# Optimization experiments

Hardware: AMD Instinct MI355X
Metric: run time of the kernel (lower is better)

Reference implementation:

```python
import jax, jax.numpy as jnp
import numpy as np

LAMBDA_GEO = 0.5


def setup_inputs() -> dict:
    key = jax.random.key(0)
    embeddings = jax.random.normal(key, (4, 2048, 512), dtype=jnp.float32)
    return {"embeddings": embeddings}


def _geometric_loss(embeddings):
    b, s, d = embeddings.shape
    x = embeddings.reshape(b * s, d)  # [N, d]
    sq_norm = jnp.sum(x * x, axis=-1)  # [N]
    sq = sq_norm[:, None] + sq_norm[None, :] - 2.0 * (x @ x.T)  # [N, N]
    sq = jnp.maximum(sq, 0.0)
    dist = jnp.sqrt(sq)  # torch.cdist(p=2)
    return jnp.mean(jnp.exp(-dist * 0.1)) * 0.1


def reference(embeddings):
    geometric_loss = _geometric_loss(embeddings)
    total_geometric = LAMBDA_GEO * geometric_loss
    return geometric_loss, total_geometric
```

## Files before the change

### kernel.cpp

```cpp
#include <hip/hip_runtime.h>

#define NROWS 8192
#define DIM   512
#define NT    64
#define NTRI  (NT * (NT + 1) / 2)
#define NACC  64

using f32x4 = __attribute__((ext_vector_type(4))) float;

__device__ __forceinline__ unsigned char f2e4m3(float x) {
    unsigned ux = __float_as_uint(x);
    unsigned s  = (ux >> 24) & 0x80u;
    float a = __uint_as_float(ux & 0x7FFFFFFFu);
    a = fminf(a, 448.0f);
    unsigned ua = __float_as_uint(a);
    int eb = (int)(ua >> 23);
    if (eb < 121) eb = 121;
    float step  = __uint_as_float((unsigned)(eb - 3) << 23);
    float istep = __uint_as_float((unsigned)(257 - eb) << 23);
    float q = rintf(a * istep) * step;
    q = fminf(q, 448.0f);
    if (q < 0.001953125f)
        return (unsigned char)s;
    unsigned uq = __float_as_uint(q);
    int eq = (int)(uq >> 23) - 127;
    unsigned byte;
    if (eq < -6) byte = (unsigned)(q * 512.0f);
    else         byte = (unsigned)((eq + 7) << 3) | ((uq >> 20) & 7u);
    return (unsigned char)(s | byte);
}

__global__ __launch_bounds__(256) void norm_convert_kernel(
    const float* __restrict__ X, unsigned char* __restrict__ Xq,
    float* __restrict__ norms, float* __restrict__ acc)
{
    const int tid  = threadIdx.x;
    const int lane = tid & 63;
    const int w    = tid >> 6;
    const int row  = blockIdx.x * 4 + w;

    if (blockIdx.x == 0 && tid < NACC) acc[tid] = 0.0f;

    const float* xr = X + (size_t)row * DIM + lane * 8;
    float4 v0 = *(const float4*)xr;
    float4 v1 = *(const float4*)(xr + 4);

    float s = 0.0f;
    s = fmaf(v0.x, v0.x, s); s = fmaf(v0.y, v0.y, s);
    s = fmaf(v0.z, v0.z, s); s = fmaf(v0.w, v0.w, s);
    s = fmaf(v1.x, v1.x, s); s = fmaf(v1.y, v1.y, s);
    s = fmaf(v1.z, v1.z, s); s = fmaf(v1.w, v1.w, s);

    union { unsigned char b[8]; uint2 v; } pk;
    pk.b[0] = f2e4m3(v0.x); pk.b[1] = f2e4m3(v0.y);
    pk.b[2] = f2e4m3(v0.z); pk.b[3] = f2e4m3(v0.w);
    pk.b[4] = f2e4m3(v1.x); pk.b[5] = f2e4m3(v1.y);
    pk.b[6] = f2e4m3(v1.z); pk.b[7] = f2e4m3(v1.w);

    const int slab = lane >> 2;
    const int cpos = (lane & 3) ^ ((row >> 2) & 3);
    *(uint2*)(Xq + (size_t)row * DIM + slab * 32 + cpos * 8) = pk.v;

    #pragma unroll
    for (int off = 32; off > 0; off >>= 1) s += __shfl_down(s, off, 64);
    if (lane == 0) norms[row] = s;
}

__global__ __launch_bounds__(256, 4) void pair_loss_gemm_kernel(
    const unsigned char* __restrict__ Xq, const float* __restrict__ norms,
    float* __restrict__ acc)
{
    __shared__ __align__(16) char As0[4096];
    __shared__ __align__(16) char As1[4096];
    __shared__ __align__(16) char Bs0[4096];
    __shared__ __align__(16) char Bs1[4096];
    __shared__ float wsum[4];

    int t = blockIdx.x, bi = 0;
    while (t >= (NT - bi)) { t -= (NT - bi); bi++; }
    const int bj = bi + t;

    const int tid  = threadIdx.x;
    const int lane = tid & 63;
    const int w    = tid >> 6;

    const int rowA = bi * 128;
    const int rowB = bj * 128;

    f32x4 accv[4][4];
    const f32x4 zero = {0.0f, 0.0f, 0.0f, 0.0f};
    #pragma unroll
    for (int a = 0; a < 4; a++)
        #pragma unroll
        for (int b = 0; b < 4; b++) accv[a][b] = zero;

    const int r0 = tid >> 1;
    const int h0 = tid & 1;
    const int wb = r0 * 32 + h0 * 16;
    const unsigned char* gA = Xq + (size_t)(rowA + r0) * DIM + h0 * 16;
    const unsigned char* gB = Xq + (size_t)(rowB + r0) * DIM + h0 * 16;

    const int fr = lane & 15;
    const int q  = lane >> 4;
    const int fo = fr * 32 + (q ^ ((fr >> 2) & 3)) * 8;
    const int wr = (w & 1) * 64;
    const int wc = (w >> 1) * 64;

    {
        uint4 pa = *(const uint4*)gA;
        uint4 pb = *(const uint4*)gB;
        *(uint4*)(As0 + wb) = pa;
        *(uint4*)(Bs0 + wb) = pb;
    }
    __syncthreads();

    char* curA = As0; char* nxtA = As1;
    char* curB = Bs0; char* nxtB = Bs1;

    #pragma unroll 1
    for (int k = 0; k < 16; k++) {
        uint4 pa, pb;
        const bool more = (k < 15);
        if (more) {
            const int k0 = (k + 1) * 32;
            pa = *(const uint4*)(gA + k0);
            pb = *(const uint4*)(gB + k0);
        }

        long af[4], bf[4];
        #pragma unroll
        for (int a = 0; a < 4; a++)
            af[a] = *(const long*)(curA + (wr + a * 16) * 32 + fo);
        #pragma unroll
        for (int b = 0; b < 4; b++)
            bf[b] = *(const long*)(curB + (wc + b * 16) * 32 + fo);

        #pragma unroll
        for (int a = 0; a < 4; a++)
            #pragma unroll
            for (int b = 0; b < 4; b++)
                accv[a][b] = __builtin_amdgcn_mfma_f32_16x16x32_fp8_fp8(
                    af[a], bf[b], accv[a][b], 0, 0, 0);

        if (more) {
            *(uint4*)(nxtA + wb) = pa;
            *(uint4*)(nxtB + wb) = pb;
            __syncthreads();
            char* tA = curA; curA = nxtA; nxtA = tA;
            char* tB = curB; curB = nxtB; nxtB = tB;
        }
    }

    const float wgt = (bi == bj) ? 1.0f : 2.0f;
    float lsum = 0.0f;
    #pragma unroll
    for (int a = 0; a < 4; a++) {
        const int gi0 = rowA + wr + a * 16 + (lane >> 4) * 4;
        #pragma unroll
        for (int b = 0; b < 4; b++) {
            const int gj = rowB + wc + b * 16 + (lane & 15);
            const float nj = norms[gj];
            #pragma unroll
            for (int r = 0; r < 4; r++) {
                const int gi = gi0 + r;
                float sq = fmaf(-2.0f, accv[a][b][r], norms[gi] + nj);
                sq = fmaxf(sq, 0.0f);
                float term = __expf(-0.1f * sqrtf(sq));
                if (gi == gj) term = 1.0f;
                lsum += term;
            }
        }
    }
    lsum *= wgt;
    #pragma unroll
    for (int off = 32; off > 0; off >>= 1) lsum += __shfl_down(lsum, off, 64);
    if (lane == 0) wsum[w] = lsum;
    __syncthreads();
    if (tid == 0)
        atomicAdd(&acc[blockIdx.x & (NACC - 1)],
                  wsum[0] + wsum[1] + wsum[2] + wsum[3]);
}

__global__ void finalize_kernel(const float* __restrict__ acc,
                                float* __restrict__ out)
{
    const int lane = threadIdx.x;
    float s = (lane < NACC) ? acc[lane] : 0.0f;
    #pragma unroll
    for (int off = 32; off > 0; off >>= 1) s += __shfl_down(s, off, 64);
    if (lane == 0) {
        const float inv = 1.0f / ((float)NROWS * (float)NROWS);
        float loss = s * inv * 0.1f;
        out[0] = loss;
        out[1] = 0.5f * loss;
    }
}

extern "C" void kernel_launch(void* const* d_in, const int* in_sizes, int n_in,
                              void* d_out, int out_size, void* d_ws, size_t ws_size,
                              hipStream_t stream)
{
    const float* X = (const float*)d_in[0];
    float* out = (float*)d_out;

    char* ws = (char*)d_ws;
    float*         acc   = (float*)ws;
    float*         norms = (float*)(ws + 1024);
    unsigned char* Xq    = (unsigned char*)(ws + 1024 + 32768);

    norm_convert_kernel<<<NROWS / 4, 256, 0, stream>>>(X, Xq, norms, acc);
    pair_loss_gemm_kernel<<<NTRI, 256, 0, stream>>>(Xq, norms, acc);
    finalize_kernel<<<1, 64, 0, stream>>>(acc, out);
}
```

Baseline: 114.4 us.

## Stage K-halves via async global-to-LDS loads with 32-chunk XOR swizzle

Replaces the 16-step register-staged double buffer with two large K-halves (256 bytes per row) loaded directly into shared memory via global_load_lds, cutting the per-step barriers down to a few. The fp8 layout written by the convert kernel changes to a 32-chunk XOR swizzle keyed on row, so fragment reads from the 256-byte LDS rows avoid bank conflicts. LDS use grows to 64KB per block, so occupancy drops to 2 blocks per CU, and loads no longer overlap compute within a half.

```diff
diff --git a/kernel.cpp b/kernel.cpp
--- a/kernel.cpp
+++ b/kernel.cpp
@@ -7,6 +7,13 @@
 #define NACC  64
 
 using f32x4 = __attribute__((ext_vector_type(4))) float;
+
+typedef __attribute__((address_space(1))) const void* as1_cvptr;
+typedef __attribute__((address_space(3))) void*       as3_vptr;
+
+__device__ __forceinline__ void async16(const void* g, void* l) {
+    __builtin_amdgcn_global_load_lds((as1_cvptr)g, (as3_vptr)l, 16, 0, 0);
+}
 
 __device__ __forceinline__ unsigned char f2e4m3(float x) {
     unsigned ux = __float_as_uint(x);
@@ -57,23 +64,22 @@
     pk.b[4] = f2e4m3(v1.x); pk.b[5] = f2e4m3(v1.y);
     pk.b[6] = f2e4m3(v1.z); pk.b[7] = f2e4m3(v1.w);
 
-    const int slab = lane >> 2;
-    const int cpos = (lane & 3) ^ ((row >> 2) & 3);
-    *(uint2*)(Xq + (size_t)row * DIM + slab * 32 + cpos * 8) = pk.v;
+    const int h    = lane >> 5;
+    const int cs   = lane & 31;
+    const int cpos = cs ^ (row & 15);
+    *(uint2*)(Xq + (size_t)row * DIM + h * 256 + cpos * 8) = pk.v;
 
     #pragma unroll
     for (int off = 32; off > 0; off >>= 1) s += __shfl_down(s, off, 64);
     if (lane == 0) norms[row] = s;
 }
 
-__global__ __launch_bounds__(256, 4) void pair_loss_gemm_kernel(
+__global__ __launch_bounds__(256, 2) void pair_loss_gemm_kernel(
     const unsigned char* __restrict__ Xq, const float* __restrict__ norms,
     float* __restrict__ acc)
 {
-    __shared__ __align__(16) char As0[4096];
-    __shared__ __align__(16) char As1[4096];
-    __shared__ __align__(16) char Bs0[4096];
-    __shared__ __align__(16) char Bs1[4096];
+    __shared__ __align__(16) char As[32768];
+    __shared__ __align__(16) char Bs[32768];
     __shared__ float wsum[4];
 
     int t = blockIdx.x, bi = 0;
@@ -94,61 +100,45 @@
         #pragma unroll
         for (int b = 0; b < 4; b++) accv[a][b] = zero;
 
-    const int r0 = tid >> 1;
-    const int h0 = tid & 1;
-    const int wb = r0 * 32 + h0 * 16;
-    const unsigned char* gA = Xq + (size_t)(rowA + r0) * DIM + h0 * 16;
-    const unsigned char* gB = Xq + (size_t)(rowB + r0) * DIM + h0 * 16;
+    const int rl = lane >> 4;
+    const int pc = lane & 15;
+    const unsigned char* gA = Xq + (size_t)(rowA + rl) * DIM + pc * 16;
+    const unsigned char* gB = Xq + (size_t)(rowB + rl) * DIM + pc * 16;
 
     const int fr = lane & 15;
     const int q  = lane >> 4;
-    const int fo = fr * 32 + (q ^ ((fr >> 2) & 3)) * 8;
     const int wr = (w & 1) * 64;
     const int wc = (w >> 1) * 64;
 
-    {
-        uint4 pa = *(const uint4*)gA;
-        uint4 pb = *(const uint4*)gB;
-        *(uint4*)(As0 + wb) = pa;
-        *(uint4*)(Bs0 + wb) = pb;
-    }
-    __syncthreads();
-
-    char* curA = As0; char* nxtA = As1;
-    char* curB = Bs0; char* nxtB = Bs1;
-
     #pragma unroll 1
-    for (int k = 0; k < 16; k++) {
-        uint4 pa, pb;
-        const bool more = (k < 15);
-        if (more) {
-            const int k0 = (k + 1) * 32;
-            pa = *(const uint4*)(gA + k0);
-            pb = *(const uint4*)(gB + k0);
+    for (int h = 0; h < 2; h++) {
+        #pragma unroll
+        for (int n = 0; n < 8; n++) {
+            const int go = h * 256 + (w * 8 + n) * 2048;
+            const int lo = (w * 8 + n) * 1024;
+            async16(gA + go, As + lo);
+            async16(gB + go, Bs + lo);
         }
-
-        long af[4], bf[4];
-        #pragma unroll
-        for (int a = 0; a < 4; a++)
-            af[a] = *(const long*)(curA + (wr + a * 16) * 32 + fo);
-        #pragma unroll
-        for (int b = 0; b < 4; b++)
-            bf[b] = *(const long*)(curB + (wc + b * 16) * 32 + fo);
-
-        #pragma unroll
-        for (int a = 0; a < 4; a++)
+        __syncthreads();
+
+        #pragma unroll
+        for (int s = 0; s < 8; s++) {
+            const int off = (((s * 4 + q) ^ fr) & 31) * 8;
+            long af[4], bf[4];
+            #pragma unroll
+            for (int a = 0; a < 4; a++)
+                af[a] = *(const long*)(As + (wr + a * 16 + fr) * 256 + off);
             #pragma unroll
             for (int b = 0; b < 4; b++)
-                accv[a][b] = __builtin_amdgcn_mfma_f32_16x16x32_fp8_fp8(
-                    af[a], bf[b], accv[a][b], 0, 0, 0);
-
-        if (more) {
-            *(uint4*)(nxtA + wb) = pa;
-            *(uint4*)(nxtB + wb) = pb;
-            __syncthreads();
-            char* tA = curA; curA = nxtA; nxtA = tA;
-            char* tB = curB; curB = nxtB; nxtB = tB;
+                bf[b] = *(const long*)(Bs + (wc + b * 16 + fr) * 256 + off);
+            #pragma unroll
+            for (int a = 0; a < 4; a++)
+                #pragma unroll
+                for (int b = 0; b < 4; b++)
+                    accv[a][b] = __builtin_amdgcn_mfma_f32_16x16x32_fp8_fp8(
+                        af[a], bf[b], accv[a][b], 0, 0, 0);
         }
+        if (h == 0) __syncthreads();
     }
 
     const float wgt = (bi == bj) ? 1.0f : 2.0f;
```

After: 114.2 us. About the same (-0.2%).
